# Optimization experiments

Measured on AMD Instinct MI355X. Metric: run time of the kernel, lower is better.

Reference implementation:

```python
import jax, jax.numpy as jnp
import numpy as np

N = 100000       # nodes
E = 3200000      # directed edges (before self-loops)
D_IN, D_H, D_OUT = 512, 128, 64


def setup_inputs() -> dict:
    key = jax.random.key(0)
    k = jax.random.split(key, 6)
    x = jax.random.normal(k[0], (N, D_IN), jnp.float32)
    edge_index = jax.random.randint(k[1], (2, E), 0, N, dtype=jnp.int32)
    # Glorot-style init, matching GCNConv's linear weights
    W1 = jax.random.normal(k[2], (D_IN, D_H), jnp.float32) * np.float32(1.0 / np.sqrt(D_IN))
    b1 = jnp.zeros((D_H,), jnp.float32)
    W2 = jax.random.normal(k[3], (D_H, D_OUT), jnp.float32) * np.float32(1.0 / np.sqrt(D_H))
    b2 = jnp.zeros((D_OUT,), jnp.float32)
    return {"x": x, "edge_index": edge_index, "W1": W1, "b1": b1, "W2": W2, "b2": b2}


def _gcn_layer(h, src, dst, norm, W, b):
    # GCNConv: transform, then normalized gather/scatter-add aggregation
    h = h @ W                                  # [N, F_out]
    msg = h[src] * norm[:, None]               # gather + per-edge scale
    agg = jax.ops.segment_sum(msg, dst, num_segments=N)  # scatter-add
    return agg + b


def reference(x, edge_index, W1, b1, W2, b2):
    # add self-loops (GCNConv default add_self_loops=True)
    loops = jnp.arange(N, dtype=edge_index.dtype)
    src = jnp.concatenate([edge_index[0], loops])
    dst = jnp.concatenate([edge_index[1], loops])
    # symmetric normalization: D^{-1/2} (A+I) D^{-1/2}
    deg = jax.ops.segment_sum(jnp.ones_like(dst, dtype=x.dtype), dst, num_segments=N)
    dinv = jax.lax.rsqrt(jnp.maximum(deg, 1.0))  # deg >= 1 because of self-loops
    norm = dinv[src] * dinv[dst]                 # per-edge weight
    h = jax.nn.relu(_gcn_layer(x, src, dst, norm, W1, b1))
    return _gcn_layer(h, src, dst, norm, W2, b2)
```

## Files before the change

### kernel.cpp

```cpp
#include <hip/hip_runtime.h>
#include <hip/hip_bf16.h>


typedef __bf16 bf16x8 __attribute__((ext_vector_type(8)));
typedef float  f32x4  __attribute__((ext_vector_type(4)));

__device__ inline unsigned rne16(float x) {
    unsigned u = __float_as_uint(x);
    return (u + 0x7fffu + ((u >> 16) & 1u)) >> 16;
}

__global__ void deg_kernel(const int* __restrict__ dst, int E, unsigned* __restrict__ deg) {
    int stride = gridDim.x * blockDim.x;
    for (int e = blockIdx.x * blockDim.x + threadIdx.x; e < E; e += stride)
        atomicAdd(&deg[dst[e]], 1u);
}

__global__ void scan_block(const unsigned* __restrict__ deg, int* __restrict__ off,
                           unsigned* __restrict__ partials, float* __restrict__ dinv, int N) {
    __shared__ unsigned s[256];
    int v = blockIdx.x * 256 + threadIdx.x;
    unsigned x = (v < N) ? deg[v] : 0u;
    s[threadIdx.x] = x;
    __syncthreads();
    #pragma unroll
    for (int d = 1; d < 256; d <<= 1) {
        unsigned t = (threadIdx.x >= d) ? s[threadIdx.x - d] : 0u;
        __syncthreads();
        s[threadIdx.x] += t;
        __syncthreads();
    }
    if (v < N) {
        off[v] = (int)(s[threadIdx.x] - x);
        dinv[v] = rsqrtf((float)(x + 1u));
    }
    if (threadIdx.x == 255) partials[blockIdx.x] = s[255];
}

__global__ void scan_partials(unsigned* __restrict__ partials, int B) {
    __shared__ unsigned s[1024];
    int i = threadIdx.x;
    unsigned x = (i < B) ? partials[i] : 0u;
    s[i] = x;
    __syncthreads();
    #pragma unroll
    for (int d = 1; d < 1024; d <<= 1) {
        unsigned t = (i >= d) ? s[i - d] : 0u;
        __syncthreads();
        s[i] += t;
        __syncthreads();
    }
    if (i < B) partials[i] = s[i] - x;
}

__global__ void add_partials(int* __restrict__ off, const unsigned* __restrict__ partials,
                             int N, int E) {
    int v = blockIdx.x * 256 + threadIdx.x;
    if (v < N) off[v] += (int)partials[blockIdx.x];
    if (v == 0) off[N] = E;
}

__global__ void fill_csr(const int* __restrict__ src, const int* __restrict__ dst, int E,
                         const int* __restrict__ off, unsigned* __restrict__ cursor,
                         int* __restrict__ csr) {
    int stride = gridDim.x * blockDim.x;
    for (int e = blockIdx.x * blockDim.x + threadIdx.x; e < E; e += stride) {
        int d = dst[e];
        unsigned p = atomicAdd(&cursor[d], 1u);
        csr[off[d] + (int)p] = src[e];
    }
}

__global__ void tsplit(const float* __restrict__ W, __bf16* __restrict__ hi,
                       __bf16* __restrict__ lo, int K, int Nc) {
    int i = blockIdx.x * 256 + threadIdx.x;
    if (i >= K * Nc) return;
    int k = i / Nc, n = i % Nc;
    float f = W[i];
    __bf16 h = (__bf16)f;
    hi[(size_t)n * K + k] = h;
    lo[(size_t)n * K + k] = (__bf16)(f - (float)h);
}

template <int BN, int K, bool SPLITA>
__global__ __launch_bounds__(256) void gemm_mfma(
    const void* __restrict__ Ap, const __bf16* __restrict__ Bhi,
    const __bf16* __restrict__ Blo, const float* __restrict__ dinv,
    __bf16* __restrict__ C, int M)
{
    constexpr int NC = BN / 16;
    const int lane = threadIdx.x & 63;
    const int wave = threadIdx.x >> 6;
    const int m0 = (blockIdx.x * 4 + wave) * 32;
    if (m0 >= M) return;
    const int lrow = lane & 15;
    const int lk = (lane >> 4) * 8;

    f32x4 acc[2][NC];
    #pragma unroll
    for (int r = 0; r < 2; ++r)
        #pragma unroll
        for (int c = 0; c < NC; ++c) acc[r][c] = (f32x4){0.f, 0.f, 0.f, 0.f};

    for (int kk = 0; kk < K; kk += 32) {
        bf16x8 ah[2], al[2];
        if (SPLITA) {
            const float* A = (const float*)Ap;
            #pragma unroll
            for (int r = 0; r < 2; ++r) {
                const float* p = A + (size_t)(m0 + r * 16 + lrow) * K + kk + lk;
                float4 f0 = *(const float4*)p;
                float4 f1 = *(const float4*)(p + 4);
                float fv[8] = {f0.x, f0.y, f0.z, f0.w, f1.x, f1.y, f1.z, f1.w};
                #pragma unroll
                for (int j = 0; j < 8; ++j) {
                    __bf16 h = (__bf16)fv[j];
                    ah[r][j] = h;
                    al[r][j] = (__bf16)(fv[j] - (float)h);
                }
            }
        } else {
            const __bf16* A = (const __bf16*)Ap;
            #pragma unroll
            for (int r = 0; r < 2; ++r)
                ah[r] = *(const bf16x8*)(A + (size_t)(m0 + r * 16 + lrow) * K + kk + lk);
        }
        #pragma unroll
        for (int c = 0; c < NC; ++c) {
            bf16x8 bh = *(const bf16x8*)(Bhi + (size_t)(c * 16 + lrow) * K + kk + lk);
            bf16x8 bl = *(const bf16x8*)(Blo + (size_t)(c * 16 + lrow) * K + kk + lk);
            #pragma unroll
            for (int r = 0; r < 2; ++r) {
                acc[r][c] = __builtin_amdgcn_mfma_f32_16x16x32_bf16(ah[r], bh, acc[r][c], 0, 0, 0);
                acc[r][c] = __builtin_amdgcn_mfma_f32_16x16x32_bf16(ah[r], bl, acc[r][c], 0, 0, 0);
                if (SPLITA)
                    acc[r][c] = __builtin_amdgcn_mfma_f32_16x16x32_bf16(al[r], bh, acc[r][c], 0, 0, 0);
            }
        }
    }
    #pragma unroll
    for (int r = 0; r < 2; ++r) {
        #pragma unroll
        for (int j = 0; j < 4; ++j) {
            int m = m0 + r * 16 + (lane >> 4) * 4 + j;
            float dv = dinv[m];
            #pragma unroll
            for (int c = 0; c < NC; ++c)
                C[(size_t)m * BN + c * 16 + (lane & 15)] = (__bf16)(acc[r][c][j] * dv);
        }
    }
}

__global__ __launch_bounds__(256) void agg128(
    const int* __restrict__ off, const int* __restrict__ csr,
    const unsigned* __restrict__ hs,
    const float* __restrict__ dinv, const float* __restrict__ bias,
    unsigned* __restrict__ h1, int N)
{
    const int lane = threadIdx.x & 63;
    const int v = blockIdx.x * 4 + (threadIdx.x >> 6);
    if (v >= N) return;
    const int s0 = off[v], s1 = off[v + 1];
    float a0 = 0.f, a1 = 0.f;
    for (int e0 = s0; e0 < s1; e0 += 64) {
        int nid = (e0 + lane < s1) ? csr[e0 + lane] : 0;
        int cnt = min(64, s1 - e0);
        int j = 0;
        for (; j + 8 <= cnt; j += 8) {
            unsigned u[8];
            #pragma unroll
            for (int q = 0; q < 8; ++q) {
                int s = __shfl(nid, j + q);
                u[q] = hs[(size_t)s * 64 + lane];
            }
            #pragma unroll
            for (int q = 0; q < 8; ++q) {
                a0 += __uint_as_float(u[q] << 16);
                a1 += __uint_as_float(u[q] & 0xffff0000u);
            }
        }
        for (; j < cnt; ++j) {
            int s = __shfl(nid, j);
            unsigned u = hs[(size_t)s * 64 + lane];
            a0 += __uint_as_float(u << 16);
            a1 += __uint_as_float(u & 0xffff0000u);
        }
    }
    unsigned su = hs[(size_t)v * 64 + lane];
    const float dv = dinv[v];
    float r0 = (a0 + __uint_as_float(su << 16)) * dv + bias[lane * 2 + 0];
    float r1 = (a1 + __uint_as_float(su & 0xffff0000u)) * dv + bias[lane * 2 + 1];
    r0 = fmaxf(r0, 0.f);
    r1 = fmaxf(r1, 0.f);
    h1[(size_t)v * 64 + lane] = rne16(r0) | (rne16(r1) << 16);
}

__global__ __launch_bounds__(256) void agg64(
    const int* __restrict__ off, const int* __restrict__ csr,
    const unsigned short* __restrict__ hs2, const float* __restrict__ dinv,
    const float* __restrict__ bias, float* __restrict__ out, int N)
{
    const int lane = threadIdx.x & 63;
    const int v = blockIdx.x * 4 + (threadIdx.x >> 6);
    if (v >= N) return;
    const int s0 = off[v], s1 = off[v + 1];
    float a0 = 0.f;
    for (int e0 = s0; e0 < s1; e0 += 64) {
        int nid = (e0 + lane < s1) ? csr[e0 + lane] : 0;
        int cnt = min(64, s1 - e0);
        int j = 0;
        for (; j + 8 <= cnt; j += 8) {
            unsigned short u[8];
            #pragma unroll
            for (int q = 0; q < 8; ++q) {
                int s = __shfl(nid, j + q);
                u[q] = hs2[(size_t)s * 64 + lane];
            }
            #pragma unroll
            for (int q = 0; q < 8; ++q)
                a0 += __uint_as_float((unsigned)u[q] << 16);
        }
        for (; j < cnt; ++j) {
            int s = __shfl(nid, j);
            a0 += __uint_as_float((unsigned)hs2[(size_t)s * 64 + lane] << 16);
        }
    }
    float self = __uint_as_float((unsigned)hs2[(size_t)v * 64 + lane] << 16);
    out[(size_t)v * 64 + lane] = (a0 + self) * dinv[v] + bias[lane];
}

extern "C" void kernel_launch(void* const* d_in, const int* in_sizes, int n_in,
                              void* d_out, int out_size, void* d_ws, size_t ws_size,
                              hipStream_t stream)
{
    const float* x  = (const float*)d_in[0];
    const int*   ei = (const int*)d_in[1];
    const float* W1 = (const float*)d_in[2];
    const float* b1 = (const float*)d_in[3];
    const float* W2 = (const float*)d_in[4];
    const float* b2 = (const float*)d_in[5];
    float* out = (float*)d_out;

    const int N = in_sizes[0] / 512;
    const int E = in_sizes[1] / 2;
    const int* src = ei;
    const int* dst = ei + E;

    unsigned* deg      = (unsigned*)d_ws;
    unsigned* cursor   = deg + N;
    int*      off      = (int*)(cursor + N);
    unsigned* partials = (unsigned*)(off + N + 4);
    float*    dinv     = (float*)(partials + 1024);
    int*      csr      = (int*)(dinv + N);
    __bf16*   Bt1hi    = (__bf16*)(csr + E);
    __bf16*   Bt1lo    = Bt1hi + 128 * 512;
    __bf16*   Bt2hi    = Bt1lo + 128 * 512;
    __bf16*   Bt2lo    = Bt2hi + 64 * 128;
    __bf16*   hs       = Bt2lo + 64 * 128;
    __bf16*   h1       = hs + (size_t)N * 128;
    __bf16*   hs2      = h1 + (size_t)N * 128;

    const int SB = (N + 255) / 256;

    hipMemsetAsync(deg, 0, (size_t)N * 8, stream);

    deg_kernel<<<dim3(2048), 256, 0, stream>>>(dst, E, deg);

    scan_block<<<dim3(SB), 256, 0, stream>>>(deg, off, partials, dinv, N);
    scan_partials<<<dim3(1), 1024, 0, stream>>>(partials, SB);
    add_partials<<<dim3(SB), 256, 0, stream>>>(off, partials, N, E);
    fill_csr<<<dim3(2048), 256, 0, stream>>>(src, dst, E, off, cursor, csr);

    tsplit<<<dim3((512 * 128 + 255) / 256), 256, 0, stream>>>(W1, Bt1hi, Bt1lo, 512, 128);
    tsplit<<<dim3((128 * 64 + 255) / 256), 256, 0, stream>>>(W2, Bt2hi, Bt2lo, 128, 64);

    gemm_mfma<128, 512, true><<<dim3((N + 127) / 128), 256, 0, stream>>>(
        x, Bt1hi, Bt1lo, dinv, hs, N);
    agg128<<<dim3((N + 3) / 4), 256, 0, stream>>>(
        off, csr, (const unsigned*)hs, dinv, b1, (unsigned*)h1, N);

    gemm_mfma<64, 128, false><<<dim3((N + 127) / 128), 256, 0, stream>>>(
        h1, Bt2hi, Bt2lo, dinv, hs2, N);
    agg64<<<dim3((N + 3) / 4), 256, 0, stream>>>(
        off, csr, (const unsigned short*)hs2, dinv, b2, out, N);
}
```

Measured before the change: 972.6 us.

## Split GEMM tiles across waves by column and share split A via LDS

The first GEMM now has each 256-thread block own 32 rows. The A tile is loaded once, split into bf16 hi/lo and staged in shared memory, and each of the four waves computes a 32-column slice. Before, each wave loaded and split its own 32 rows against all 128 columns. The second GEMM partitions 64 rows by 2 column halves across waves and adds bounds clamping. The intent is more blocks, fewer registers per wave and better occupancy, at the cost of two barriers per k-step and repeated B loads per block.

```diff
diff --git a/kernel.cpp b/kernel.cpp
--- a/kernel.cpp
+++ b/kernel.cpp
@@ -3,6 +3,7 @@
 
 
 typedef __bf16 bf16x8 __attribute__((ext_vector_type(8)));
+typedef __bf16 bf16x4 __attribute__((ext_vector_type(4)));
 typedef float  f32x4  __attribute__((ext_vector_type(4)));
 
 __device__ inline unsigned rne16(float x) {
@@ -82,59 +83,62 @@
     lo[(size_t)n * K + k] = (__bf16)(f - (float)h);
 }
 
-template <int BN, int K, bool SPLITA>
-__global__ __launch_bounds__(256) void gemm_mfma(
-    const void* __restrict__ Ap, const __bf16* __restrict__ Bhi,
+template <int K>
+__global__ __launch_bounds__(256) void gemm1_mfma(
+    const float* __restrict__ A, const __bf16* __restrict__ Bhi,
     const __bf16* __restrict__ Blo, const float* __restrict__ dinv,
     __bf16* __restrict__ C, int M)
 {
-    constexpr int NC = BN / 16;
-    const int lane = threadIdx.x & 63;
-    const int wave = threadIdx.x >> 6;
-    const int m0 = (blockIdx.x * 4 + wave) * 32;
-    if (m0 >= M) return;
+    constexpr int LDA = 40;
+    __shared__ __bf16 shi[32][LDA];
+    __shared__ __bf16 slo[32][LDA];
+
+    const int tid = threadIdx.x;
+    const int lane = tid & 63;
+    const int wave = tid >> 6;
+    const int m0 = blockIdx.x * 32;
+    const int col0 = wave * 32;
     const int lrow = lane & 15;
     const int lk = (lane >> 4) * 8;
-
-    f32x4 acc[2][NC];
+    const int arow = tid >> 3;
+    const int ac4 = (tid & 7) * 4;
+
+    f32x4 acc[2][2];
     #pragma unroll
     for (int r = 0; r < 2; ++r)
         #pragma unroll
-        for (int c = 0; c < NC; ++c) acc[r][c] = (f32x4){0.f, 0.f, 0.f, 0.f};
-
+        for (int c = 0; c < 2; ++c) acc[r][c] = (f32x4){0.f, 0.f, 0.f, 0.f};
+
+    #pragma unroll 1
     for (int kk = 0; kk < K; kk += 32) {
+        __syncthreads();
+        {
+            int gr = m0 + arow; if (gr >= M) gr = M - 1;
+            float4 f = *(const float4*)(A + (size_t)gr * K + kk + ac4);
+            bf16x4 h, l;
+            h[0] = (__bf16)f.x; l[0] = (__bf16)(f.x - (float)h[0]);
+            h[1] = (__bf16)f.y; l[1] = (__bf16)(f.y - (float)h[1]);
+            h[2] = (__bf16)f.z; l[2] = (__bf16)(f.z - (float)h[2]);
+            h[3] = (__bf16)f.w; l[3] = (__bf16)(f.w - (float)h[3]);
+            *(bf16x4*)&shi[arow][ac4] = h;
+            *(bf16x4*)&slo[arow][ac4] = l;
+        }
+        __syncthreads();
         bf16x8 ah[2], al[2];
-        if (SPLITA) {
-            const float* A = (const float*)Ap;
-            #pragma unroll
-            for (int r = 0; r < 2; ++r) {
-                const float* p = A + (size_t)(m0 + r * 16 + lrow) * K + kk + lk;
-                float4 f0 = *(const float4*)p;
-                float4 f1 = *(const float4*)(p + 4);
-                float fv[8] = {f0.x, f0.y, f0.z, f0.w, f1.x, f1.y, f1.z, f1.w};
-                #pragma unroll
-                for (int j = 0; j < 8; ++j) {
-                    __bf16 h = (__bf16)fv[j];
-                    ah[r][j] = h;
-                    al[r][j] = (__bf16)(fv[j] - (float)h);
-                }
-            }
-        } else {
-            const __bf16* A = (const __bf16*)Ap;
-            #pragma unroll
-            for (int r = 0; r < 2; ++r)
-                ah[r] = *(const bf16x8*)(A + (size_t)(m0 + r * 16 + lrow) * K + kk + lk);
-        }
-        #pragma unroll
-        for (int c = 0; c < NC; ++c) {
-            bf16x8 bh = *(const bf16x8*)(Bhi + (size_t)(c * 16 + lrow) * K + kk + lk);
-            bf16x8 bl = *(const bf16x8*)(Blo + (size_t)(c * 16 + lrow) * K + kk + lk);
+        #pragma unroll
+        for (int r = 0; r < 2; ++r) {
+            ah[r] = *(const bf16x8*)&shi[r * 16 + lrow][lk];
+            al[r] = *(const bf16x8*)&slo[r * 16 + lrow][lk];
+        }
+        #pragma unroll
+        for (int c = 0; c < 2; ++c) {
+            bf16x8 bh = *(const bf16x8*)(Bhi + (size_t)(col0 + c * 16 + lrow) * K + kk + lk);
+            bf16x8 bl = *(const bf16x8*)(Blo + (size_t)(col0 + c * 16 + lrow) * K + kk + lk);
             #pragma unroll
             for (int r = 0; r < 2; ++r) {
                 acc[r][c] = __builtin_amdgcn_mfma_f32_16x16x32_bf16(ah[r], bh, acc[r][c], 0, 0, 0);
                 acc[r][c] = __builtin_amdgcn_mfma_f32_16x16x32_bf16(ah[r], bl, acc[r][c], 0, 0, 0);
-                if (SPLITA)
-                    acc[r][c] = __builtin_amdgcn_mfma_f32_16x16x32_bf16(al[r], bh, acc[r][c], 0, 0, 0);
+                acc[r][c] = __builtin_amdgcn_mfma_f32_16x16x32_bf16(al[r], bh, acc[r][c], 0, 0, 0);
             }
         }
     }
@@ -143,10 +147,63 @@
         #pragma unroll
         for (int j = 0; j < 4; ++j) {
             int m = m0 + r * 16 + (lane >> 4) * 4 + j;
+            if (m >= M) continue;
             float dv = dinv[m];
             #pragma unroll
-            for (int c = 0; c < NC; ++c)
-                C[(size_t)m * BN + c * 16 + (lane & 15)] = (__bf16)(acc[r][c][j] * dv);
+            for (int c = 0; c < 2; ++c)
+                C[(size_t)m * 128 + col0 + c * 16 + lrow] = (__bf16)(acc[r][c][j] * dv);
+        }
+    }
+}
+
+template <int K>
+__global__ __launch_bounds__(256) void gemm2_mfma(
+    const __bf16* __restrict__ A, const __bf16* __restrict__ Bhi,
+    const __bf16* __restrict__ Blo, const float* __restrict__ dinv,
+    __bf16* __restrict__ C, int M)
+{
+    const int lane = threadIdx.x & 63;
+    const int wave = threadIdx.x >> 6;
+    const int m0 = blockIdx.x * 64 + (wave >> 1) * 32;
+    const int col0 = (wave & 1) * 32;
+    const int lrow = lane & 15;
+    const int lk = (lane >> 4) * 8;
+
+    f32x4 acc[2][2];
+    #pragma unroll
+    for (int r = 0; r < 2; ++r)
+        #pragma unroll
+        for (int c = 0; c < 2; ++c) acc[r][c] = (f32x4){0.f, 0.f, 0.f, 0.f};
+
+    #pragma unroll
+    for (int kk = 0; kk < K; kk += 32) {
+        bf16x8 ah[2];
+        #pragma unroll
+        for (int r = 0; r < 2; ++r) {
+            int gr = m0 + r * 16 + lrow; if (gr >= M) gr = M - 1;
+            ah[r] = *(const bf16x8*)(A + (size_t)gr * K + kk + lk);
+        }
+        #pragma unroll
+        for (int c = 0; c < 2; ++c) {
+            bf16x8 bh = *(const bf16x8*)(Bhi + (size_t)(col0 + c * 16 + lrow) * K + kk + lk);
+            bf16x8 bl = *(const bf16x8*)(Blo + (size_t)(col0 + c * 16 + lrow) * K + kk + lk);
+            #pragma unroll
+            for (int r = 0; r < 2; ++r) {
+                acc[r][c] = __builtin_amdgcn_mfma_f32_16x16x32_bf16(ah[r], bh, acc[r][c], 0, 0, 0);
+                acc[r][c] = __builtin_amdgcn_mfma_f32_16x16x32_bf16(ah[r], bl, acc[r][c], 0, 0, 0);
+            }
+        }
+    }
+    #pragma unroll
+    for (int r = 0; r < 2; ++r) {
+        #pragma unroll
+        for (int j = 0; j < 4; ++j) {
+            int m = m0 + r * 16 + (lane >> 4) * 4 + j;
+            if (m >= M) continue;
+            float dv = dinv[m];
+            #pragma unroll
+            for (int c = 0; c < 2; ++c)
+                C[(size_t)m * 64 + col0 + c * 16 + lrow] = (__bf16)(acc[r][c][j] * dv);
         }
     }
 }
@@ -274,13 +331,11 @@
     tsplit<<<dim3((512 * 128 + 255) / 256), 256, 0, stream>>>(W1, Bt1hi, Bt1lo, 512, 128);
     tsplit<<<dim3((128 * 64 + 255) / 256), 256, 0, stream>>>(W2, Bt2hi, Bt2lo, 128, 64);
 
-    gemm_mfma<128, 512, true><<<dim3((N + 127) / 128), 256, 0, stream>>>(
-        x, Bt1hi, Bt1lo, dinv, hs, N);
+    gemm1_mfma<512><<<dim3((N + 31) / 32), 256, 0, stream>>>(x, Bt1hi, Bt1lo, dinv, hs, N);
     agg128<<<dim3((N + 3) / 4), 256, 0, stream>>>(
         off, csr, (const unsigned*)hs, dinv, b1, (unsigned*)h1, N);
 
-    gemm_mfma<64, 128, false><<<dim3((N + 127) / 128), 256, 0, stream>>>(
-        h1, Bt2hi, Bt2lo, dinv, hs2, N);
+    gemm2_mfma<128><<<dim3((N + 63) / 64), 256, 0, stream>>>(h1, Bt2hi, Bt2lo, dinv, hs2, N);
     agg64<<<dim3((N + 3) / 4), 256, 0, stream>>>(
         off, csr, (const unsigned short*)hs2, dinv, b2, out, N);
 }
```

New measurement: 967.1 us. No clear change (-0.6%).
